# Optimization experiments

Hardware: AMD Instinct MI355X
Metric: run time of the kernel (lower is better)

The kernel has to match this reference:

```python
import jax, jax.numpy as jnp
import numpy as np

BS, D, L, H = 8, 256, 1024, 8
DK = D // H
EPS = 1e-8


def setup_inputs() -> dict:
    key = jax.random.key(0)
    ks = jax.random.split(key, 9)
    queries = jax.random.normal(ks[0], (BS, D, L), jnp.float32)
    keys = jax.random.normal(ks[1], (BS, D, L), jnp.float32)
    values = jax.random.normal(ks[2], (BS, D, L), jnp.float32)
    # binary float mask over positions, (bs, L, 1) as the module expects
    mask = (jax.random.uniform(ks[3], (BS, L, 1)) > 0.1).astype(jnp.float32)
    # grouped 1x1 conv weights: one (dk, dk) block per head (xavier-ish scale)
    wscale = np.sqrt(2.0 / (DK + DK)).astype(np.float32)
    Wq = jax.random.normal(ks[4], (H, DK, DK), jnp.float32) * wscale
    Wk = jax.random.normal(ks[5], (H, DK, DK), jnp.float32) * wscale
    Wv = jax.random.normal(ks[6], (H, DK, DK), jnp.float32) * wscale
    # full 1x1 conv projection
    Wp = jax.random.normal(ks[7], (D, D), jnp.float32) * np.sqrt(1.0 / D).astype(np.float32)
    bp = jnp.zeros((D,), jnp.float32)
    return {"queries": queries, "keys": keys, "values": values, "mask": mask,
            "Wq": Wq, "Wk": Wk, "Wv": Wv, "Wp": Wp, "bp": bp}


def _grouped_conv1x1(x, W):
    # x: (bs, D, L) viewed as (bs, H, dk, L); W: (H, dk_out, dk_in)
    bs, _, l = x.shape
    xh = x.reshape(bs, H, DK, l)
    return jnp.einsum('hij,bhjl->bhil', W, xh)  # (bs, H, dk, L)


def _masked_softmax(logits, mask4):
    # logits: (bs, H, L, L); mask4: (bs, 1, 1, L) -- faithful to module's custom softmax
    max_value = jax.lax.stop_gradient(jnp.max(logits * mask4, axis=-1, keepdims=True))
    z = (logits - max_value) * mask4
    m = jnp.exp(z) * mask4
    n = jnp.sum(m, axis=-1, keepdims=True)
    p_mask = mask4 * jnp.swapaxes(mask4, 2, 3)  # (bs, 1, L, L)
    return p_mask * (m / (n + EPS))


def reference(queries, keys, values, mask, Wq, Wk, Wv, Wp, bp):
    bs, c, l = queries.shape
    m = jnp.swapaxes(mask, 1, 2)          # (bs, 1, L)
    m4 = m[:, :, None, :]                  # (bs, 1, 1, L)
    q = _grouped_conv1x1(queries, Wq) * m4  # (bs, H, dk, L)
    k = _grouped_conv1x1(keys, Wk) * m4
    v = _grouped_conv1x1(values, Wv)
    # attn[b,h,d,e] = sum_c q[b,h,c,d] k[b,h,c,e]  (no 1/sqrt(dk) scaling, as in source)
    attn = jnp.einsum('bhcd,bhce->bhde', q, k)
    atn = _masked_softmax(attn, m4)
    # value[b,h,c,k] = sum_d atn[b,h,k,d] * (v*mask)[b,h,c,d]
    val = jnp.einsum('bhkd,bhcd->bhck', atn, v * m4)
    val = val.reshape(bs, c, l)
    out = jnp.einsum('ij,bjl->bil', Wp, val) + bp[None, :, None]
    return jnp.swapaxes(out * m, 1, 2)      # (bs, L, D)
```

## Files before the change

### kernel.cpp

```cpp
#include <hip/hip_runtime.h>
#include <math.h>


constexpr int cD  = 256;
constexpr int cL  = 1024;
constexpr int cH  = 8;
constexpr int cDK = 32;

typedef _Float16 f16;
typedef __attribute__((ext_vector_type(8))) _Float16 h8;
typedef __attribute__((ext_vector_type(4))) _Float16 h4;
typedef __attribute__((ext_vector_type(4))) float f4v;

__global__ __launch_bounds__(256, 4) void proj_qkv_kernel(
    const float* __restrict__ queries, const float* __restrict__ keys,
    const float* __restrict__ values, const float* __restrict__ mask,
    const float* __restrict__ Wq, const float* __restrict__ Wk,
    const float* __restrict__ Wv, f16* __restrict__ qp_h,
    f16* __restrict__ kp_h, f16* __restrict__ vp_h)
{
    const int t    = threadIdx.x;
    const int bid  = blockIdx.x;
    const int lt   = bid & 15;
    const int bh   = bid >> 4;
    const int h    = bh & 7;
    const int b    = bh >> 3;
    const int l0   = lt * 64;
    const int lane = t & 63, w = t >> 6, ln15 = lane & 15, lq = lane >> 4;
    const int l    = l0 + w * 16 + ln15;

    const float mk = mask[b * cL + l];
    const size_t xbase = ((size_t)(b * cD + h * cDK)) * cL + l;
    const int    wbase = h * cDK * cDK + lq * 8;

    const float* Xs[3] = {queries, keys, values};
    const float* Ws[3] = {Wq, Wk, Wv};
    f4v d0[3], d1[3];

    #pragma unroll
    for (int m = 0; m < 3; ++m) {
        const float* __restrict__ X = Xs[m];
        const float* __restrict__ W = Ws[m];
        h8 bx, a0, a1;
        #pragma unroll
        for (int i = 0; i < 8; ++i)
            bx[i] = (f16)X[xbase + (size_t)(lq * 8 + i) * cL];
        #pragma unroll
        for (int i = 0; i < 8; ++i) {
            a0[i] = (f16)W[wbase + ln15 * cDK + i];
            a1[i] = (f16)W[wbase + (16 + ln15) * cDK + i];
        }
        f4v z = {0.f, 0.f, 0.f, 0.f};
        d0[m] = __builtin_amdgcn_mfma_f32_16x16x32_f16(a0, bx, z, 0, 0, 0);
        d1[m] = __builtin_amdgcn_mfma_f32_16x16x32_f16(a1, bx, z, 0, 0, 0);
    }

    {
        const size_t qb = ((size_t)bh * cL + l) * cDK;
        h4 o0, o1;
        #pragma unroll
        for (int i = 0; i < 4; ++i) { o0[i] = (f16)d0[0][i]; o1[i] = (f16)d1[0][i]; }
        *reinterpret_cast<h4*>(&qp_h[qb + lq * 4])      = o0;
        *reinterpret_cast<h4*>(&qp_h[qb + 16 + lq * 4]) = o1;
    }
    {
        const size_t kb = ((size_t)bh * cL + l) * cDK;
        h4 o0, o1;
        #pragma unroll
        for (int i = 0; i < 4; ++i) {
            o0[i] = (f16)(d0[1][i] * mk);
            o1[i] = (f16)(d1[1][i] * mk);
        }
        *reinterpret_cast<h4*>(&kp_h[kb + lq * 4])      = o0;
        *reinterpret_cast<h4*>(&kp_h[kb + 16 + lq * 4]) = o1;
    }
    {
        const size_t vb = (size_t)bh * cDK * cL + l;
        #pragma unroll
        for (int i = 0; i < 4; ++i) {
            vp_h[vb + (size_t)(lq * 4 + i) * cL]      = (f16)d0[2][i];
            vp_h[vb + (size_t)(16 + lq * 4 + i) * cL] = (f16)d1[2][i];
        }
    }
}

__global__ __launch_bounds__(256, 5) void attn_kernel(
    const float* __restrict__ mask, const f16* __restrict__ qp_h,
    const f16* __restrict__ kp_h, const f16* __restrict__ vp_h,
    f16* __restrict__ val_h)
{
    __shared__ __align__(16) char smem[28672];
    f16* ks  = (f16*)smem;
    f16* vsb = (f16*)(smem + 10240);
    f16* pbf = (f16*)(smem + 19456);

    const int t     = threadIdx.x;
    const int bid   = blockIdx.x;
    const int strip = bid & 15;
    const int bh    = bid >> 4;
    const int b     = bh >> 3;
    const int r0    = strip * 64;
    const int lane  = t & 63;
    const int w     = t >> 6;
    const int ln15  = lane & 15;
    const int lq    = lane >> 4;

    const size_t kvbase = ((size_t)bh) * 32768;
    const int se = t >> 2, sb = (t & 3) * 8;
    const int vc = t >> 3, veb = (t & 7) * 8;

    const h8 qf = *reinterpret_cast<const h8*>(
        &qp_h[((size_t)bh * cL + r0 + w * 16 + ln15) * cDK + lq * 8]);

    {
        h8 kh = *reinterpret_cast<const h8*>(&kp_h[kvbase + se * 32 + sb]);
        *reinterpret_cast<h8*>(&ks[se * 40 + sb]) = kh;
        h8 vv = *reinterpret_cast<const h8*>(&vp_h[kvbase + vc * 1024 + veb]);
        *reinterpret_cast<h8*>(&vsb[vc * 72 + veb]) = vv;
    }

    f4v o0 = {0.f, 0.f, 0.f, 0.f}, o1 = {0.f, 0.f, 0.f, 0.f};
    float mo = -INFINITY, lrp = 0.f;
    const int prow  = (w * 16 + ln15) * 72;
    const int vsoff = ln15 * 72 + lq * 8;

    for (int et = 0; et < 16; ++et) {
        __syncthreads();
        const int pp = et & 1;
        const bool pre = (et < 15);
        h8 khp, vvp;
        if (pre) {
            const int e0n = (et + 1) * 64;
            khp = *reinterpret_cast<const h8*>(&kp_h[kvbase + (e0n + se) * 32 + sb]);
            vvp = *reinterpret_cast<const h8*>(&vp_h[kvbase + vc * 1024 + e0n + veb]);
        }
        float4 mk4[4];
        #pragma unroll
        for (int es = 0; es < 4; ++es)
            mk4[es] = *reinterpret_cast<const float4*>(
                &mask[b * cL + et * 64 + es * 16 + lq * 4]);

        f4v sA[4];
        #pragma unroll
        for (int es = 0; es < 4; ++es) {
            const h8 kf = *reinterpret_cast<const h8*>(
                &ks[pp * 2560 + (es * 16 + ln15) * 40 + lq * 8]);
            f4v z = {0.f, 0.f, 0.f, 0.f};
            sA[es] = __builtin_amdgcn_mfma_f32_16x16x32_f16(kf, qf, z, 0, 0, 0);
        }

        float tm = fmaxf(fmaxf(fmaxf(sA[0][0], sA[0][1]), fmaxf(sA[0][2], sA[0][3])),
                   fmaxf(fmaxf(fmaxf(sA[1][0], sA[1][1]), fmaxf(sA[1][2], sA[1][3])),
                   fmaxf(fmaxf(fmaxf(sA[2][0], sA[2][1]), fmaxf(sA[2][2], sA[2][3])),
                         fmaxf(fmaxf(sA[3][0], sA[3][1]), fmaxf(sA[3][2], sA[3][3])))));
        tm = fmaxf(tm, __shfl_xor(tm, 16));
        tm = fmaxf(tm, __shfl_xor(tm, 32));
        const float mn = fmaxf(mo, tm);
        const float al = __expf(mo - mn);
        mo = mn;
        o0[0] *= al; o0[1] *= al; o0[2] *= al; o0[3] *= al;
        o1[0] *= al; o1[1] *= al; o1[2] *= al; o1[3] *= al;

        float ps = 0.f;
        #pragma unroll
        for (int es = 0; es < 4; ++es) {
            float p0 = mk4[es].x * __expf(sA[es][0] - mn);
            float p1 = mk4[es].y * __expf(sA[es][1] - mn);
            float p2 = mk4[es].z * __expf(sA[es][2] - mn);
            float p3 = mk4[es].w * __expf(sA[es][3] - mn);
            ps += (p0 + p1) + (p2 + p3);
            h4 pk; pk[0] = (f16)p0; pk[1] = (f16)p1; pk[2] = (f16)p2; pk[3] = (f16)p3;
            *reinterpret_cast<h4*>(&pbf[prow + es * 16 + lq * 4]) = pk;
        }
        lrp = lrp * al + ps;

        #pragma unroll
        for (int ch = 0; ch < 2; ++ch) {
            h8 pf  = *reinterpret_cast<const h8*>(&pbf[prow + ch * 32 + lq * 8]);
            h8 va0 = *reinterpret_cast<const h8*>(&vsb[pp * 2304 + vsoff + ch * 32]);
            h8 va1 = *reinterpret_cast<const h8*>(&vsb[pp * 2304 + vsoff + ch * 32 + 1152]);
            o0 = __builtin_amdgcn_mfma_f32_16x16x32_f16(va0, pf, o0, 0, 0, 0);
            o1 = __builtin_amdgcn_mfma_f32_16x16x32_f16(va1, pf, o1, 0, 0, 0);
        }

        if (pre) {
            *reinterpret_cast<h8*>(&ks[(pp ^ 1) * 2560 + se * 40 + sb]) = khp;
            *reinterpret_cast<h8*>(&vsb[(pp ^ 1) * 2304 + vc * 72 + veb]) = vvp;
        }
    }

    {
        float lr = lrp;
        lr += __shfl_xor(lr, 16);
        lr += __shfl_xor(lr, 32);
        const float linv = 1.0f / (lr + 1e-8f);
        const int h = bh & 7;
        const size_t obase = ((size_t)(b * cL + r0 + w * 16 + ln15)) * cD + h * cDK;
        h4 q0, q1;
        #pragma unroll
        for (int i = 0; i < 4; ++i) {
            q0[i] = (f16)(o0[i] * linv);
            q1[i] = (f16)(o1[i] * linv);
        }
        *reinterpret_cast<h4*>(&val_h[obase + lq * 4])      = q0;
        *reinterpret_cast<h4*>(&val_h[obase + 16 + lq * 4]) = q1;
    }
}

__global__ __launch_bounds__(256, 2) void outproj_kernel(
    const f16* __restrict__ val_h, const float* __restrict__ Wp,
    const float* __restrict__ bp, const float* __restrict__ mask,
    float* __restrict__ out)
{
    __shared__ __align__(16) f16 vt[64 * 264];
    __shared__ __align__(16) f16 wpb[64 * 264];
    __shared__ float mrow[64];

    const int t    = threadIdx.x;
    const int bid  = blockIdx.x;
    const int it   = bid & 3;
    const int lt   = (bid >> 2) & 15;
    const int b    = bid >> 6;
    const int l0   = lt * 64, i0 = it * 64;
    const int lane = t & 63, w = t >> 6, ln15 = lane & 15, lq = lane >> 4;

    {
        int row = t & 63, seg = (t >> 6) * 64;
        const f16* src = &val_h[((size_t)(b * cL + l0 + row)) * cD + seg];
        #pragma unroll
        for (int k = 0; k < 8; ++k)
            *reinterpret_cast<h8*>(&vt[row * 264 + seg + k * 8]) =
                *reinterpret_cast<const h8*>(src + k * 8);
    }
    {
        int row = t & 63, seg = (t >> 6) * 64;
        const float* src = &Wp[((size_t)(i0 + row)) * cD + seg];
        #pragma unroll
        for (int k = 0; k < 8; ++k) {
            float4 f0 = *reinterpret_cast<const float4*>(src + k * 8);
            float4 f1 = *reinterpret_cast<const float4*>(src + k * 8 + 4);
            h8 hv;
            hv[0] = (f16)f0.x; hv[1] = (f16)f0.y; hv[2] = (f16)f0.z; hv[3] = (f16)f0.w;
            hv[4] = (f16)f1.x; hv[5] = (f16)f1.y; hv[6] = (f16)f1.z; hv[7] = (f16)f1.w;
            *reinterpret_cast<h8*>(&wpb[row * 264 + seg + k * 8]) = hv;
        }
    }
    if (t < 64) mrow[t] = mask[b * cL + l0 + t];
    __syncthreads();

    f4v acc[4] = {{0.f, 0.f, 0.f, 0.f}, {0.f, 0.f, 0.f, 0.f},
                  {0.f, 0.f, 0.f, 0.f}, {0.f, 0.f, 0.f, 0.f}};
    #pragma unroll
    for (int kc = 0; kc < 8; ++kc) {
        h8 aA = *reinterpret_cast<const h8*>(&vt[(w * 16 + ln15) * 264 + kc * 32 + lq * 8]);
        #pragma unroll
        for (int ti = 0; ti < 4; ++ti) {
            h8 bB = *reinterpret_cast<const h8*>(&wpb[(ti * 16 + ln15) * 264 + kc * 32 + lq * 8]);
            acc[ti] = __builtin_amdgcn_mfma_f32_16x16x32_f16(aA, bB, acc[ti], 0, 0, 0);
        }
    }

    float mk[4];
    #pragma unroll
    for (int rg = 0; rg < 4; ++rg) mk[rg] = mrow[w * 16 + lq * 4 + rg];
    #pragma unroll
    for (int ti = 0; ti < 4; ++ti) {
        float bpv = bp[i0 + ti * 16 + ln15];
        #pragma unroll
        for (int rg = 0; rg < 4; ++rg) {
            int l = l0 + w * 16 + lq * 4 + rg;
            out[((size_t)(b * cL + l)) * cD + i0 + ti * 16 + ln15] =
                (acc[ti][rg] + bpv) * mk[rg];
        }
    }
}

extern "C" void kernel_launch(void* const* d_in, const int* in_sizes, int n_in,
                              void* d_out, int out_size, void* d_ws, size_t ws_size,
                              hipStream_t stream) {
    const float* queries = (const float*)d_in[0];
    const float* keys    = (const float*)d_in[1];
    const float* values  = (const float*)d_in[2];
    const float* mask    = (const float*)d_in[3];
    const float* Wq      = (const float*)d_in[4];
    const float* Wk      = (const float*)d_in[5];
    const float* Wv      = (const float*)d_in[6];
    const float* Wp      = (const float*)d_in[7];
    const float* bp      = (const float*)d_in[8];
    float* out = (float*)d_out;

    char* wsb = (char*)d_ws;
    f16* qp_h  = (f16*)(wsb);
    f16* kp_h  = (f16*)(wsb + (4u << 20));
    f16* vp_h  = (f16*)(wsb + (8u << 20));
    f16* val_h = (f16*)(wsb + (12u << 20));

    proj_qkv_kernel<<<dim3(1024), dim3(256), 0, stream>>>(
        queries, keys, values, mask, Wq, Wk, Wv, qp_h, kp_h, vp_h);
    attn_kernel<<<dim3(1024), dim3(256), 0, stream>>>(
        mask, qp_h, kp_h, vp_h, val_h);
    outproj_kernel<<<dim3(512), dim3(256), 0, stream>>>(val_h, Wp, bp, mask, out);
}
```

Baseline: 127.3 us.

## Drop LDS staging in output projection and reorder block index mapping

The output projection kernel no longer stages val and Wp tiles in shared memory. Each wave now loads its A fragments straight from global memory and converts Wp rows to fp16 in registers. The tile shrinks to 16 rows by 128 columns per block, so twice as many blocks are launched and the occupancy hint rises. Separately, the projection and attention kernels swap block index decoding so consecutive blocks cover different batch-head pairs rather than strips of the same one, which changes cache and scheduling locality. The cost is redundant global reads of Wp across blocks, served from L2, and less reuse per block.

```diff
diff --git a/kernel.cpp b/kernel.cpp
--- a/kernel.cpp
+++ b/kernel.cpp
@@ -21,8 +21,8 @@
 {
     const int t    = threadIdx.x;
     const int bid  = blockIdx.x;
-    const int lt   = bid & 15;
-    const int bh   = bid >> 4;
+    const int bh   = bid & 63;
+    const int lt   = bid >> 6;
     const int h    = bh & 7;
     const int b    = bh >> 3;
     const int l0   = lt * 64;
@@ -96,8 +96,8 @@
 
     const int t     = threadIdx.x;
     const int bid   = blockIdx.x;
-    const int strip = bid & 15;
-    const int bh    = bid >> 4;
+    const int bh    = bid & 63;
+    const int strip = bid >> 6;
     const int b     = bh >> 3;
     const int r0    = strip * 64;
     const int lane  = t & 63;
@@ -207,70 +207,48 @@
     }
 }
 
-__global__ __launch_bounds__(256, 2) void outproj_kernel(
+__global__ __launch_bounds__(256, 4) void outproj_kernel(
     const f16* __restrict__ val_h, const float* __restrict__ Wp,
     const float* __restrict__ bp, const float* __restrict__ mask,
     float* __restrict__ out)
 {
-    __shared__ __align__(16) f16 vt[64 * 264];
-    __shared__ __align__(16) f16 wpb[64 * 264];
-    __shared__ float mrow[64];
-
     const int t    = threadIdx.x;
     const int bid  = blockIdx.x;
-    const int it   = bid & 3;
-    const int lt   = (bid >> 2) & 15;
-    const int b    = bid >> 6;
-    const int l0   = lt * 64, i0 = it * 64;
+    const int ih   = bid & 1;
+    const int lt   = (bid >> 1) & 63;
+    const int b    = bid >> 7;
+    const int l0   = lt * 16;
     const int lane = t & 63, w = t >> 6, ln15 = lane & 15, lq = lane >> 4;
-
-    {
-        int row = t & 63, seg = (t >> 6) * 64;
-        const f16* src = &val_h[((size_t)(b * cL + l0 + row)) * cD + seg];
-        #pragma unroll
-        for (int k = 0; k < 8; ++k)
-            *reinterpret_cast<h8*>(&vt[row * 264 + seg + k * 8]) =
-                *reinterpret_cast<const h8*>(src + k * 8);
-    }
-    {
-        int row = t & 63, seg = (t >> 6) * 64;
-        const float* src = &Wp[((size_t)(i0 + row)) * cD + seg];
-        #pragma unroll
-        for (int k = 0; k < 8; ++k) {
-            float4 f0 = *reinterpret_cast<const float4*>(src + k * 8);
-            float4 f1 = *reinterpret_cast<const float4*>(src + k * 8 + 4);
-            h8 hv;
-            hv[0] = (f16)f0.x; hv[1] = (f16)f0.y; hv[2] = (f16)f0.z; hv[3] = (f16)f0.w;
-            hv[4] = (f16)f1.x; hv[5] = (f16)f1.y; hv[6] = (f16)f1.z; hv[7] = (f16)f1.w;
-            *reinterpret_cast<h8*>(&wpb[row * 264 + seg + k * 8]) = hv;
-        }
-    }
-    if (t < 64) mrow[t] = mask[b * cL + l0 + t];
-    __syncthreads();
-
-    f4v acc[4] = {{0.f, 0.f, 0.f, 0.f}, {0.f, 0.f, 0.f, 0.f},
-                  {0.f, 0.f, 0.f, 0.f}, {0.f, 0.f, 0.f, 0.f}};
+    const int i0   = ih * 128 + w * 32;
+
+    h8 af[8];
+    const f16* vrow = &val_h[((size_t)(b * cL + l0 + ln15)) * cD + lq * 8];
     #pragma unroll
-    for (int kc = 0; kc < 8; ++kc) {
-        h8 aA = *reinterpret_cast<const h8*>(&vt[(w * 16 + ln15) * 264 + kc * 32 + lq * 8]);
-        #pragma unroll
-        for (int ti = 0; ti < 4; ++ti) {
-            h8 bB = *reinterpret_cast<const h8*>(&wpb[(ti * 16 + ln15) * 264 + kc * 32 + lq * 8]);
-            acc[ti] = __builtin_amdgcn_mfma_f32_16x16x32_f16(aA, bB, acc[ti], 0, 0, 0);
-        }
-    }
-
-    float mk[4];
+    for (int kc = 0; kc < 8; ++kc)
+        af[kc] = *reinterpret_cast<const h8*>(vrow + kc * 32);
+
+    const float4 mk4 = *reinterpret_cast<const float4*>(&mask[b * cL + l0 + lq * 4]);
+    const float mks[4] = {mk4.x, mk4.y, mk4.z, mk4.w};
+
     #pragma unroll
-    for (int rg = 0; rg < 4; ++rg) mk[rg] = mrow[w * 16 + lq * 4 + rg];
-    #pragma unroll
-    for (int ti = 0; ti < 4; ++ti) {
-        float bpv = bp[i0 + ti * 16 + ln15];
-        #pragma unroll
-        for (int rg = 0; rg < 4; ++rg) {
-            int l = l0 + w * 16 + lq * 4 + rg;
-            out[((size_t)(b * cL + l)) * cD + i0 + ti * 16 + ln15] =
-                (acc[ti][rg] + bpv) * mk[rg];
+    for (int nt = 0; nt < 2; ++nt) {
+        const int i = i0 + nt * 16 + ln15;
+        const float* wrow = &Wp[(size_t)i * cD + lq * 8];
+        f4v acc = {0.f, 0.f, 0.f, 0.f};
+        #pragma unroll
+        for (int kc = 0; kc < 8; ++kc) {
+            float4 f0 = *reinterpret_cast<const float4*>(wrow + kc * 32);
+            float4 f1 = *reinterpret_cast<const float4*>(wrow + kc * 32 + 4);
+            h8 bf;
+            bf[0] = (f16)f0.x; bf[1] = (f16)f0.y; bf[2] = (f16)f0.z; bf[3] = (f16)f0.w;
+            bf[4] = (f16)f1.x; bf[5] = (f16)f1.y; bf[6] = (f16)f1.z; bf[7] = (f16)f1.w;
+            acc = __builtin_amdgcn_mfma_f32_16x16x32_f16(af[kc], bf, acc, 0, 0, 0);
+        }
+        const float bpv = bp[i];
+        #pragma unroll
+        for (int reg = 0; reg < 4; ++reg) {
+            const int l = l0 + lq * 4 + reg;
+            out[((size_t)(b * cL + l)) * cD + i] = (acc[reg] + bpv) * mks[reg];
         }
     }
 }
@@ -299,5 +277,5 @@
         queries, keys, values, mask, Wq, Wk, Wv, qp_h, kp_h, vp_h);
     attn_kernel<<<dim3(1024), dim3(256), 0, stream>>>(
         mask, qp_h, kp_h, vp_h, val_h);
-    outproj_kernel<<<dim3(512), dim3(256), 0, stream>>>(val_h, Wp, bp, mask, out);
-}
+    outproj_kernel<<<dim3(1024), dim3(256), 0, stream>>>(val_h, Wp, bp, mask, out);
+}
```

Result: slower. 139.2 us (+9.3%).
